# Performance work log

Hardware: AMD Instinct MI355X
Metric: run time of the kernel (lower is better)

Reference implementation:

```python
import jax, jax.numpy as jnp
import numpy as np

# Faithful JAX reference for MVLiftingModule.lift_2D_to_3D with lifting_method='mean'.
# Torch semantics: for each batch, view, and part p in [1, parts_nb[b]] (in order),
# scatter-write the (weighted softmax) pixel prediction into each point that any
# Since each pixel's predicted part is unique (argmax), the winning pixel per point
# is the one maximizing key = pred_class * H*W + flat_pixel_index. We compute that
# deterministically via scatter-max, then gather features and voint-mean over views.

def setup_inputs() -> dict:
    key = jax.random.key(0)
    k1, k2, k3, k4, k5 = jax.random.split(key, 5)
    B, N, V, C, H, W = 4, 2048, 12, 50, 128, 128
    points = jax.random.normal(k1, (B, N, 3), dtype=jnp.float32)
    predictions_2d = jax.random.normal(k2, (B, V, C, H, W), dtype=jnp.float32)
    # -1 marks background pixels (no point), as in pytorch3d pix_to_face
    rendered_pix_to_point = jax.random.randint(k3, (B, V, 1, H, W), -1, N, dtype=jnp.int32)
    views_weights = jax.random.uniform(k4, (B, V, 1, 1, 1), dtype=jnp.float32)
    parts_nb = jax.random.randint(k5, (B,), 1, 7, dtype=jnp.int32)
    return {"points": points, "predictions_2d": predictions_2d,
            "rendered_pix_to_point": rendered_pix_to_point,
            "views_weights": views_weights, "parts_nb": parts_nb}


def reference(points, predictions_2d, rendered_pix_to_point, views_weights, parts_nb):
    B, N, _ = points.shape
    _, V, C, H, W = predictions_2d.shape
    P = H * W

    p2p = rendered_pix_to_point[:, :, 0]            # (B,V,H,W)
    valid = p2p != -1                                # pix_to_face_mask
    idx = jnp.where(valid, p2p % N, 0)               # invalid pixels -> point 0 (as in torch)

    probs = jax.nn.softmax(predictions_2d, axis=2)   # softmax over classes
    pred_max = jnp.argmax(probs, axis=2).astype(jnp.int32)   # (B,V,H,W)
    feats = (views_weights * probs).reshape(B, V, C, P)       # weighted predictions

    # pixel participates iff valid and its predicted part in [1, parts_nb[b]]
    mask_pix = valid & (pred_max >= 1) & (pred_max <= parts_nb[:, None, None, None])
    mask_pix = mask_pix.reshape(B, V, P)
    idx_f = idx.reshape(B, V, P)

    pix = jnp.arange(P, dtype=jnp.int32)
    kkey = pred_max.reshape(B, V, P) * P + pix
    kkey = jnp.where(mask_pix, kkey, -1)

    bi = jnp.arange(B)[:, None, None]
    vi = jnp.arange(V)[None, :, None]
    winner = jnp.full((B, V, N), -1, dtype=jnp.int32).at[bi, vi, idx_f].max(kkey)

    voints_mask = (winner >= 0)                      # (B,V,N)
    win_pix = jnp.where(voints_mask, winner % P, 0)  # winning pixel per point/view

    # gather weighted features at winning pixel: (B,V,C,N)
    point_feats = jnp.take_along_axis(feats, win_pix[:, :, None, :], axis=3)
    m = voints_mask.astype(feats.dtype)
    masked = point_feats * m[:, :, None, :]

    # vointmean: masked mean over views -> (B,C,N)
    denom = jnp.maximum(m.sum(axis=1), 1.0)          # (B,N)
    labels_3d_feats = masked.sum(axis=1) / denom[:, None, :]
    return labels_3d_feats
```

## Files before the change

kernel.cpp:

```cpp
#include <hip/hip_runtime.h>

#define B 4
#define N 2048
#define V 12
#define C 50
#define HH 128
#define WW 128
#define P (HH*WW)

__global__ __launch_bounds__(256) void k1_argmax_scatter(
    const float4* __restrict__ predv,
    const int4*  __restrict__ p2pv,
    const int*   __restrict__ parts_nb,
    int*         __restrict__ winner) {
  const int PQ = P / 4;
  int t = blockIdx.x * 256 + threadIdx.x;
  if (t >= B * V * PQ) return;
  int q  = t % PQ;
  int bv = t / PQ;
  int b  = bv / V;

  size_t base = (size_t)bv * C * PQ + q;
  float4 x = predv[base];
  float b0 = x.x, b1 = x.y, b2 = x.z, b3 = x.w;
  int   a0 = 0,  a1 = 0,  a2 = 0,  a3 = 0;
  for (int c = 1; c < C; ++c) {
    float4 y = predv[base + (size_t)c * PQ];
    if (y.x > b0) { b0 = y.x; a0 = c; }
    if (y.y > b1) { b1 = y.y; a1 = c; }
    if (y.z > b2) { b2 = y.z; a2 = c; }
    if (y.w > b3) { b3 = y.w; a3 = c; }
  }

  int4 pt = p2pv[(size_t)bv * PQ + q];
  int pn = parts_nb[b];
  int p0 = q * 4;
  int* wbase = winner + bv * N;
  if (pt.x != -1 && a0 >= 1 && a0 <= pn) atomicMax(wbase + pt.x, a0 * P + p0);
  if (pt.y != -1 && a1 >= 1 && a1 <= pn) atomicMax(wbase + pt.y, a1 * P + p0 + 1);
  if (pt.z != -1 && a2 >= 1 && a2 <= pn) atomicMax(wbase + pt.z, a2 * P + p0 + 2);
  if (pt.w != -1 && a3 >= 1 && a3 <= pn) atomicMax(wbase + pt.w, a3 * P + p0 + 3);
}

__global__ __launch_bounds__(256) void k2_gather(
    const float* __restrict__ pred,
    const int*   __restrict__ winner,
    const float* __restrict__ vw,
    float*       __restrict__ out) {
  int wid  = blockIdx.x * (256 / 64) + (threadIdx.x >> 6);
  int lane = threadIdx.x & 63;
  if (wid >= B * N) return;
  int b = wid / N;
  int n = wid - b * N;

  float acc = 0.f;
  int cnt = 0;
  for (int v = 0; v < V; ++v) {
    int wv = winner[(b * V + v) * N + n];
    if (wv < 0) continue;
    cnt++;
    int wp = wv & (P - 1);
    float logit = -3.0e38f;
    if (lane < C)
      logit = pred[(((size_t)(b * V + v)) * C + lane) * P + wp];
    float m = logit;
    #pragma unroll
    for (int off = 32; off > 0; off >>= 1) m = fmaxf(m, __shfl_xor(m, off));
    float e = (lane < C) ? expf(logit - m) : 0.f;
    float s = e;
    #pragma unroll
    for (int off = 32; off > 0; off >>= 1) s += __shfl_xor(s, off);
    acc += e * (vw[b * V + v] / s);
  }
  float denom = (float)(cnt > 0 ? cnt : 1);
  if (lane < C)
    out[((size_t)b * C + lane) * N + n] = acc / denom;
}

extern "C" void kernel_launch(void* const* d_in, const int* in_sizes, int n_in,
                              void* d_out, int out_size, void* d_ws, size_t ws_size,
                              hipStream_t stream) {
  const float* pred  = (const float*)d_in[1];
  const int*   p2p   = (const int*)d_in[2];
  const float* vw    = (const float*)d_in[3];
  const int*   parts = (const int*)d_in[4];
  float* out = (float*)d_out;
  int* winner = (int*)d_ws;

  hipMemsetAsync(winner, 0xFF, (size_t)B * V * N * sizeof(int), stream);

  int nthreads1 = B * V * (P / 4);
  k1_argmax_scatter<<<(nthreads1 + 255) / 256, 256, 0, stream>>>(
      (const float4*)pred, (const int4*)p2p, parts, winner);

  k2_gather<<<(B * N) / 4, 256, 0, stream>>>(pred, winner, vw, out);
}
```

Measured before the change: 269.9 us.

## Precompute softmax denominators in argmax pass and unroll gather over views

The argmax kernel now also accumulates the sum of exponentials of the logits for each pixel and writes it to workspace. The gather kernel reads that denominator directly instead of doing two wave-wide shuffle reductions per view. It also loads all view winners up front and unrolls the view loop branch-free so the per-view loads can overlap. The cost is extra exp work and a stores pass in the first kernel, plus no max-subtraction in the softmax, which can overflow for large logits.

```diff
diff --git a/kernel.cpp b/kernel.cpp
--- a/kernel.cpp
+++ b/kernel.cpp
@@ -4,15 +4,14 @@
 #define N 2048
 #define V 12
 #define C 50
-#define HH 128
-#define WW 128
-#define P (HH*WW)
+#define P 16384
 
 __global__ __launch_bounds__(256) void k1_argmax_scatter(
     const float4* __restrict__ predv,
     const int4*  __restrict__ p2pv,
     const int*   __restrict__ parts_nb,
-    int*         __restrict__ winner) {
+    int*         __restrict__ winner,
+    float4*      __restrict__ sexp) {
   const int PQ = P / 4;
   int t = blockIdx.x * 256 + threadIdx.x;
   if (t >= B * V * PQ) return;
@@ -22,15 +21,19 @@
 
   size_t base = (size_t)bv * C * PQ + q;
   float4 x = predv[base];
-  float b0 = x.x, b1 = x.y, b2 = x.z, b3 = x.w;
+  float m0 = x.x, m1 = x.y, m2 = x.z, m3 = x.w;
+  float s0 = __expf(x.x), s1 = __expf(x.y), s2 = __expf(x.z), s3 = __expf(x.w);
   int   a0 = 0,  a1 = 0,  a2 = 0,  a3 = 0;
   for (int c = 1; c < C; ++c) {
     float4 y = predv[base + (size_t)c * PQ];
-    if (y.x > b0) { b0 = y.x; a0 = c; }
-    if (y.y > b1) { b1 = y.y; a1 = c; }
-    if (y.z > b2) { b2 = y.z; a2 = c; }
-    if (y.w > b3) { b3 = y.w; a3 = c; }
+    if (y.x > m0) { m0 = y.x; a0 = c; }
+    if (y.y > m1) { m1 = y.y; a1 = c; }
+    if (y.z > m2) { m2 = y.z; a2 = c; }
+    if (y.w > m3) { m3 = y.w; a3 = c; }
+    s0 += __expf(y.x); s1 += __expf(y.y);
+    s2 += __expf(y.z); s3 += __expf(y.w);
   }
+  sexp[(size_t)bv * PQ + q] = make_float4(s0, s1, s2, s3);
 
   int4 pt = p2pv[(size_t)bv * PQ + q];
   int pn = parts_nb[b];
@@ -45,32 +48,30 @@
 __global__ __launch_bounds__(256) void k2_gather(
     const float* __restrict__ pred,
     const int*   __restrict__ winner,
+    const float* __restrict__ sexp,
     const float* __restrict__ vw,
     float*       __restrict__ out) {
   int wid  = blockIdx.x * (256 / 64) + (threadIdx.x >> 6);
   int lane = threadIdx.x & 63;
-  if (wid >= B * N) return;
-  int b = wid / N;
-  int n = wid - b * N;
+  int b = wid >> 11;
+  int n = wid & (N - 1);
+
+  int wv[V];
+  #pragma unroll
+  for (int v = 0; v < V; ++v) wv[v] = winner[(b * V + v) * N + n];
 
   float acc = 0.f;
   int cnt = 0;
+  #pragma unroll
   for (int v = 0; v < V; ++v) {
-    int wv = winner[(b * V + v) * N + n];
-    if (wv < 0) continue;
-    cnt++;
-    int wp = wv & (P - 1);
-    float logit = -3.0e38f;
-    if (lane < C)
-      logit = pred[(((size_t)(b * V + v)) * C + lane) * P + wp];
-    float m = logit;
-    #pragma unroll
-    for (int off = 32; off > 0; off >>= 1) m = fmaxf(m, __shfl_xor(m, off));
-    float e = (lane < C) ? expf(logit - m) : 0.f;
-    float s = e;
-    #pragma unroll
-    for (int off = 32; off > 0; off >>= 1) s += __shfl_xor(s, off);
-    acc += e * (vw[b * V + v] / s);
+    bool valid = wv[v] >= 0;
+    int wp = valid ? (wv[v] & (P - 1)) : 0;
+    size_t bvo = (size_t)(b * V + v);
+    float l = (lane < C) ? pred[(bvo * C + lane) * P + wp] : 0.f;
+    float s = sexp[bvo * P + wp];
+    float w = vw[b * V + v] / s;
+    cnt += valid ? 1 : 0;
+    acc += valid ? __expf(l) * w : 0.f;
   }
   float denom = (float)(cnt > 0 ? cnt : 1);
   if (lane < C)
@@ -85,13 +86,15 @@
   const float* vw    = (const float*)d_in[3];
   const int*   parts = (const int*)d_in[4];
   float* out = (float*)d_out;
-  int* winner = (int*)d_ws;
+
+  int*   winner = (int*)d_ws;
+  float* sexp   = (float*)((char*)d_ws + (size_t)B * V * N * sizeof(int));
 
   hipMemsetAsync(winner, 0xFF, (size_t)B * V * N * sizeof(int), stream);
 
   int nthreads1 = B * V * (P / 4);
   k1_argmax_scatter<<<(nthreads1 + 255) / 256, 256, 0, stream>>>(
-      (const float4*)pred, (const int4*)p2p, parts, winner);
+      (const float4*)pred, (const int4*)p2p, parts, winner, (float4*)sexp);
 
-  k2_gather<<<(B * N) / 4, 256, 0, stream>>>(pred, winner, vw, out);
+  k2_gather<<<(B * N) / 4, 256, 0, stream>>>(pred, winner, sexp, vw, out);
 }
```

Result: no change. 270.3 us (+0.1%).
